# Optimization experiments

Measured on AMD Instinct MI355X. Metric: run time of the kernel, lower is better.

Reference implementation:

```python
import jax, jax.numpy as jnp
import numpy as np

NUM_EXPERTS = 64
TOP_K = 8
ALPHA = 0.001


def setup_inputs() -> dict:
    key = jax.random.key(0)
    k1, k2 = jax.random.split(key)
    hidden_states = jax.random.normal(k1, (16384, 2048), dtype=jnp.float32)
    # nn.Linear(D, E) weight has shape (E, D); init ~ N(0, 1/sqrt(D))
    weight = jax.random.normal(k2, (NUM_EXPERTS, 2048), dtype=jnp.float32) / jnp.sqrt(2048.0)
    return {"hidden_states": hidden_states, "weight": weight}


def reference(hidden_states, weight):
    # Router logits: (N, E)
    logits = jnp.einsum("nd,ed->ne", hidden_states, weight)
    scores = jax.nn.softmax(logits, axis=-1)

    # top-k (lax.top_k returns sorted values; torch used sorted=False, same set)
    topk_weights, topk_indices = jax.lax.top_k(scores, TOP_K)  # (N, K)
    topk_weights = topk_weights / jnp.sum(topk_weights, axis=-1, keepdims=True)

    # Aux load-balancing loss (training path). Instead of materializing a
    # (N, K, E) one-hot tensor, count tokens per expert with a scatter-add.
    num_tokens = hidden_states.shape[0]
    counts = jnp.zeros((NUM_EXPERTS,), dtype=jnp.float32).at[topk_indices.ravel()].add(1.0)
    tokens_per_expert = counts / (num_tokens * TOP_K)
    mean_prob = jnp.mean(scores, axis=0)  # (E,)
    aux_loss = ALPHA * NUM_EXPERTS * jnp.sum(tokens_per_expert * mean_prob)

    return topk_weights, topk_indices, aux_loss
```

## Files before the change

### kernel.cpp

```cpp
#include <hip/hip_runtime.h>
#include <hip/hip_bf16.h>

#define N_TOKENS 16384
#define DIM      2048
#define NEXP     64
#define TOPK     8
#define BK       32

__global__ __launch_bounds__(256) void gemm_kernel(const float* __restrict__ A,
                                                   const float* __restrict__ W,
                                                   float* __restrict__ out,
                                                   int k_len) {
    __shared__ float As[BK][260];
    __shared__ float Bs[BK][68];

    const int tid = threadIdx.x;
    const int r = tid >> 3;
    const int c = tid & 7;
    const int token_base = blockIdx.x * 256;
    const int k_start = blockIdx.y * k_len;
    out += (size_t)blockIdx.y * N_TOKENS * NEXP;

    float acc[8][8] = {};

    for (int k0 = k_start; k0 < k_start + k_len; k0 += BK) {
        #pragma unroll
        for (int l = 0; l < 8; ++l) {
            int slot = tid + l * 256;
            int row  = slot >> 3;
            int kq   = (slot & 7) * 4;
            float4 v = *(const float4*)(A + (size_t)(token_base + row) * DIM + k0 + kq);
            As[kq + 0][row] = v.x; As[kq + 1][row] = v.y;
            As[kq + 2][row] = v.z; As[kq + 3][row] = v.w;
        }
        #pragma unroll
        for (int l = 0; l < 2; ++l) {
            int slot = tid + l * 256;
            int row  = slot >> 3;
            int kq   = (slot & 7) * 4;
            float4 v = *(const float4*)(W + (size_t)row * DIM + k0 + kq);
            Bs[kq + 0][row] = v.x; Bs[kq + 1][row] = v.y;
            Bs[kq + 2][row] = v.z; Bs[kq + 3][row] = v.w;
        }
        __syncthreads();

        #pragma unroll 8
        for (int kk = 0; kk < BK; ++kk) {
            float4 a0 = *(const float4*)&As[kk][8 * r];
            float4 a1 = *(const float4*)&As[kk][8 * r + 4];
            float4 b0 = *(const float4*)&Bs[kk][8 * c];
            float4 b1 = *(const float4*)&Bs[kk][8 * c + 4];
            float a[8] = {a0.x, a0.y, a0.z, a0.w, a1.x, a1.y, a1.z, a1.w};
            float b[8] = {b0.x, b0.y, b0.z, b0.w, b1.x, b1.y, b1.z, b1.w};
            #pragma unroll
            for (int i = 0; i < 8; ++i)
                #pragma unroll
                for (int j = 0; j < 8; ++j)
                    acc[i][j] += a[i] * b[j];
        }
        __syncthreads();
    }

    #pragma unroll
    for (int i = 0; i < 8; ++i) {
        float* orow = out + (size_t)(token_base + 8 * r + i) * NEXP + 8 * c;
        *(float4*)(orow)     = make_float4(acc[i][0], acc[i][1], acc[i][2], acc[i][3]);
        *(float4*)(orow + 4) = make_float4(acc[i][4], acc[i][5], acc[i][6], acc[i][7]);
    }
}

__global__ __launch_bounds__(256) void topk_kernel(const float* __restrict__ logits,
                                                   int nslab,
                                                   float* __restrict__ out_w,
                                                   float* __restrict__ out_i,
                                                   float* __restrict__ cnt_ws,
                                                   float* __restrict__ sp_ws) {
    __shared__ float s_cnt[NEXP];
    __shared__ float s_sp[NEXP];
    if (threadIdx.x < NEXP) { s_cnt[threadIdx.x] = 0.f; s_sp[threadIdx.x] = 0.f; }
    __syncthreads();

    const int lane = threadIdx.x & 63;
    const int wave = blockIdx.x * 4 + (threadIdx.x >> 6);

    float sp  = 0.f;
    float cnt = 0.f;

    for (int t = wave; t < N_TOKENS; t += 4096) {
        float lg = 0.f;
        for (int s = 0; s < nslab; ++s)
            lg += logits[(size_t)s * N_TOKENS * NEXP + (size_t)t * NEXP + lane];

        float m = lg;
        #pragma unroll
        for (int off = 32; off; off >>= 1) m = fmaxf(m, __shfl_xor(m, off));
        float e = expf(lg - m);
        float ssum = e;
        #pragma unroll
        for (int off = 32; off; off >>= 1) ssum += __shfl_xor(ssum, off);
        float score = e / ssum;
        sp += score;

        int rank = 0;
        #pragma unroll
        for (int j = 0; j < 64; ++j) {
            float sj = __shfl(score, j);
            rank += (sj > score) || (sj == score && j < lane);
        }
        bool sel = rank < TOPK;

        float v = sel ? score : 0.f;
        #pragma unroll
        for (int off = 32; off; off >>= 1) v += __shfl_xor(v, off);

        if (sel) {
            out_w[(size_t)t * TOPK + rank] = score / v;
            out_i[(size_t)t * TOPK + rank] = (float)lane;
            cnt += 1.f;
        }
    }

    atomicAdd(&s_sp[lane], sp);
    atomicAdd(&s_cnt[lane], cnt);
    __syncthreads();
    if (threadIdx.x < 64)       atomicAdd(&cnt_ws[threadIdx.x], s_cnt[threadIdx.x]);
    else if (threadIdx.x < 128) atomicAdd(&sp_ws[threadIdx.x - 64], s_sp[threadIdx.x - 64]);
}

__global__ void finalize_kernel(const float* __restrict__ cnt_ws,
                                const float* __restrict__ sp_ws,
                                float* __restrict__ out_aux) {
    int lane = threadIdx.x;
    float v = (cnt_ws[lane] / (float)(N_TOKENS * TOPK)) *
              (sp_ws[lane] / (float)N_TOKENS);
    #pragma unroll
    for (int off = 32; off; off >>= 1) v += __shfl_xor(v, off);
    if (lane == 0) out_aux[0] = 0.001f * (float)NEXP * v;
}

extern "C" void kernel_launch(void* const* d_in, const int* in_sizes, int n_in,
                              void* d_out, int out_size, void* d_ws, size_t ws_size,
                              hipStream_t stream) {
    const float* A = (const float*)d_in[0];
    const float* W = (const float*)d_in[1];
    float* out = (float*)d_out;

    const size_t logits_elems = (size_t)N_TOKENS * NEXP;
    const size_t logits_bytes = logits_elems * sizeof(float);

    int nslab = 1;
    if (ws_size >= 8 * logits_bytes + 1024)      nslab = 8;
    else if (ws_size >= 4 * logits_bytes + 1024) nslab = 4;
    else if (ws_size >= 2 * logits_bytes + 1024) nslab = 2;

    float* l0     = (float*)d_ws;
    float* cnt_ws = (float*)((char*)d_ws + (size_t)nslab * logits_bytes);
    float* sp_ws  = cnt_ws + NEXP;

    hipMemsetAsync(cnt_ws, 0, 2 * NEXP * sizeof(float), stream);

    hipLaunchKernelGGL(gemm_kernel, dim3(N_TOKENS / 256, nslab), dim3(256), 0, stream,
                       A, W, l0, DIM / nslab);

    float* out_w = out;
    float* out_i = out + (size_t)N_TOKENS * TOPK;
    float* out_a = out + 2 * (size_t)N_TOKENS * TOPK;

    hipLaunchKernelGGL(topk_kernel, dim3(1024), dim3(256), 0, stream,
                       l0, nslab, out_w, out_i, cnt_ws, sp_ws);

    hipLaunchKernelGGL(finalize_kernel, dim3(1), dim3(64), 0, stream,
                       cnt_ws, sp_ws, out_a);
}
```

Baseline: 261.5 us.

## Enlarge GEMM token tile to 512 with padded LDS layout and deeper split-K

The GEMM block now covers 512 tokens with BK=16, and each thread computes a 16x8 accumulator tile, so every loaded weight value is reused across more rows. Shared-memory stores use a padded, grouped layout to cut bank conflicts, and global loads are issued into registers before the LDS writes. Split-K defaults to at least 4 slabs (up to 16) to keep the grid filling the GPU, and the top-k kernel sums the slabs with four independent accumulators. The cost is more register pressure from the 128 accumulators, plus more logits traffic and a larger workspace for the extra slabs; if the workspace is smaller than four slabs, the writes overrun it.

Result: slower. 272.5 us (+4.2%).

```diff
diff --git a/kernel.cpp b/kernel.cpp
--- a/kernel.cpp
+++ b/kernel.cpp
@@ -5,55 +5,80 @@
 #define DIM      2048
 #define NEXP     64
 #define TOPK     8
-#define BK       32
-
-__global__ __launch_bounds__(256) void gemm_kernel(const float* __restrict__ A,
-                                                   const float* __restrict__ W,
-                                                   float* __restrict__ out,
-                                                   int k_len) {
-    __shared__ float As[BK][260];
-    __shared__ float Bs[BK][68];
+#define BK       16
+#define TM       512
+#define APLANE   644
+#define BPLANE   100
+
+__global__ __launch_bounds__(256, 2) void gemm_kernel(const float* __restrict__ A,
+                                                      const float* __restrict__ W,
+                                                      float* __restrict__ out,
+                                                      int k_len) {
+    __shared__ float As[BK * APLANE];
+    __shared__ float Bs[BK * BPLANE];
 
     const int tid = threadIdx.x;
-    const int r = tid >> 3;
-    const int c = tid & 7;
-    const int token_base = blockIdx.x * 256;
+    const int tg  = tid >> 3;
+    const int cg  = tid & 7;
+    const int token_base = blockIdx.x * TM;
     const int k_start = blockIdx.y * k_len;
     out += (size_t)blockIdx.y * N_TOKENS * NEXP;
 
-    float acc[8][8] = {};
+    float acc[16][8] = {};
 
     for (int k0 = k_start; k0 < k_start + k_len; k0 += BK) {
+        float4 av[8];
         #pragma unroll
         for (int l = 0; l < 8; ++l) {
             int slot = tid + l * 256;
-            int row  = slot >> 3;
-            int kq   = (slot & 7) * 4;
-            float4 v = *(const float4*)(A + (size_t)(token_base + row) * DIM + k0 + kq);
-            As[kq + 0][row] = v.x; As[kq + 1][row] = v.y;
-            As[kq + 2][row] = v.z; As[kq + 3][row] = v.w;
-        }
-        #pragma unroll
-        for (int l = 0; l < 2; ++l) {
+            int row  = slot >> 2;
+            int kq   = (slot & 3) << 2;
+            av[l] = *(const float4*)(A + (size_t)(token_base + row) * DIM + k0 + kq);
+        }
+        float4 bv;
+        {
+            int row = tid >> 2;
+            int kq  = (tid & 3) << 2;
+            bv = *(const float4*)(W + (size_t)row * DIM + k0 + kq);
+        }
+
+        #pragma unroll
+        for (int l = 0; l < 8; ++l) {
             int slot = tid + l * 256;
-            int row  = slot >> 3;
-            int kq   = (slot & 7) * 4;
-            float4 v = *(const float4*)(W + (size_t)row * DIM + k0 + kq);
-            Bs[kq + 0][row] = v.x; Bs[kq + 1][row] = v.y;
-            Bs[kq + 2][row] = v.z; Bs[kq + 3][row] = v.w;
+            int row  = slot >> 2;
+            int kq   = (slot & 3) << 2;
+            float* dst = As + (row >> 4) * 20 + (row & 15);
+            dst[(kq + 0) * APLANE] = av[l].x;
+            dst[(kq + 1) * APLANE] = av[l].y;
+            dst[(kq + 2) * APLANE] = av[l].z;
+            dst[(kq + 3) * APLANE] = av[l].w;
+        }
+        {
+            int row = tid >> 2;
+            int kq  = (tid & 3) << 2;
+            float* dst = Bs + (row >> 3) * 12 + (row & 7);
+            dst[(kq + 0) * BPLANE] = bv.x;
+            dst[(kq + 1) * BPLANE] = bv.y;
+            dst[(kq + 2) * BPLANE] = bv.z;
+            dst[(kq + 3) * BPLANE] = bv.w;
         }
         __syncthreads();
 
-        #pragma unroll 8
+        #pragma unroll 4
         for (int kk = 0; kk < BK; ++kk) {
-            float4 a0 = *(const float4*)&As[kk][8 * r];
-            float4 a1 = *(const float4*)&As[kk][8 * r + 4];
-            float4 b0 = *(const float4*)&Bs[kk][8 * c];
-            float4 b1 = *(const float4*)&Bs[kk][8 * c + 4];
-            float a[8] = {a0.x, a0.y, a0.z, a0.w, a1.x, a1.y, a1.z, a1.w};
-            float b[8] = {b0.x, b0.y, b0.z, b0.w, b1.x, b1.y, b1.z, b1.w};
+            const float* ap = As + kk * APLANE + tg * 20;
+            const float* bp = Bs + kk * BPLANE + cg * 12;
+            float4 a0 = *(const float4*)(ap);
+            float4 a1 = *(const float4*)(ap + 4);
+            float4 a2 = *(const float4*)(ap + 8);
+            float4 a3 = *(const float4*)(ap + 12);
+            float4 b0 = *(const float4*)(bp);
+            float4 b1 = *(const float4*)(bp + 4);
+            float a[16] = {a0.x, a0.y, a0.z, a0.w, a1.x, a1.y, a1.z, a1.w,
+                           a2.x, a2.y, a2.z, a2.w, a3.x, a3.y, a3.z, a3.w};
+            float b[8]  = {b0.x, b0.y, b0.z, b0.w, b1.x, b1.y, b1.z, b1.w};
             #pragma unroll
-            for (int i = 0; i < 8; ++i)
+            for (int i = 0; i < 16; ++i)
                 #pragma unroll
                 for (int j = 0; j < 8; ++j)
                     acc[i][j] += a[i] * b[j];
@@ -62,8 +87,8 @@
     }
 
     #pragma unroll
-    for (int i = 0; i < 8; ++i) {
-        float* orow = out + (size_t)(token_base + 8 * r + i) * NEXP + 8 * c;
+    for (int i = 0; i < 16; ++i) {
+        float* orow = out + (size_t)(token_base + tg * 16 + i) * NEXP + cg * 8;
         *(float4*)(orow)     = make_float4(acc[i][0], acc[i][1], acc[i][2], acc[i][3]);
         *(float4*)(orow + 4) = make_float4(acc[i][4], acc[i][5], acc[i][6], acc[i][7]);
     }
@@ -82,14 +107,21 @@
 
     const int lane = threadIdx.x & 63;
     const int wave = blockIdx.x * 4 + (threadIdx.x >> 6);
+    const size_t slab_stride = (size_t)N_TOKENS * NEXP;
 
     float sp  = 0.f;
     float cnt = 0.f;
 
     for (int t = wave; t < N_TOKENS; t += 4096) {
-        float lg = 0.f;
-        for (int s = 0; s < nslab; ++s)
-            lg += logits[(size_t)s * N_TOKENS * NEXP + (size_t)t * NEXP + lane];
+        const float* p = logits + (size_t)t * NEXP + lane;
+        float s0 = 0.f, s1 = 0.f, s2 = 0.f, s3 = 0.f;
+        for (int s = 0; s < nslab; s += 4) {
+            s0 += p[(size_t)(s + 0) * slab_stride];
+            s1 += p[(size_t)(s + 1) * slab_stride];
+            s2 += p[(size_t)(s + 2) * slab_stride];
+            s3 += p[(size_t)(s + 3) * slab_stride];
+        }
+        float lg = (s0 + s1) + (s2 + s3);
 
         float m = lg;
         #pragma unroll
@@ -148,10 +180,9 @@
     const size_t logits_elems = (size_t)N_TOKENS * NEXP;
     const size_t logits_bytes = logits_elems * sizeof(float);
 
-    int nslab = 1;
-    if (ws_size >= 8 * logits_bytes + 1024)      nslab = 8;
-    else if (ws_size >= 4 * logits_bytes + 1024) nslab = 4;
-    else if (ws_size >= 2 * logits_bytes + 1024) nslab = 2;
+    int nslab = 4;
+    if (ws_size >= 16 * logits_bytes + 1024)     nslab = 16;
+    else if (ws_size >= 8 * logits_bytes + 1024) nslab = 8;
 
     float* l0     = (float*)d_ws;
     float* cnt_ws = (float*)((char*)d_ws + (size_t)nslab * logits_bytes);
@@ -159,7 +190,7 @@
 
     hipMemsetAsync(cnt_ws, 0, 2 * NEXP * sizeof(float), stream);
 
-    hipLaunchKernelGGL(gemm_kernel, dim3(N_TOKENS / 256, nslab), dim3(256), 0, stream,
+    hipLaunchKernelGGL(gemm_kernel, dim3(N_TOKENS / TM, nslab), dim3(256), 0, stream,
                        A, W, l0, DIM / nslab);
 
     float* out_w = out;
```

## Prefetch GEMM tiles into registers, raise split-K to 16 slabs, widen top-k grid

Applied to the files above, without the earlier changes.

The GEMM now loads the next K-tile into registers while the current tile is computed from shared memory, overlapping global latency with FMA work. BK is halved and launch bounds request 4 blocks per CU for occupancy. The split-K default rises from 8 to 16 slabs when the workspace allows, which gives more blocks but doubles the partial-logit traffic. The top-k kernel reduces slabs with four independent accumulators and launches twice as many blocks. The 4-way unrolled slab reduction assumes nslab is a multiple of 4, which the new host logic guarantees.

After: 282.8 us. +8.1%, slower.

```diff
diff --git a/kernel.cpp b/kernel.cpp
--- a/kernel.cpp
+++ b/kernel.cpp
@@ -5,46 +5,61 @@
 #define DIM      2048
 #define NEXP     64
 #define TOPK     8
-#define BK       32
+#define BK       16
+#define TM       256
+#define NSLAB    16
 
-__global__ __launch_bounds__(256) void gemm_kernel(const float* __restrict__ A,
-                                                   const float* __restrict__ W,
-                                                   float* __restrict__ out,
-                                                   int k_len) {
+__global__ __launch_bounds__(256, 4) void gemm_kernel(const float* __restrict__ A,
+                                                      const float* __restrict__ W,
+                                                      float* __restrict__ out,
+                                                      int k_len) {
     __shared__ float As[BK][260];
     __shared__ float Bs[BK][68];
 
     const int tid = threadIdx.x;
     const int r = tid >> 3;
     const int c = tid & 7;
-    const int token_base = blockIdx.x * 256;
+    const int token_base = blockIdx.x * TM;
     const int k_start = blockIdx.y * k_len;
     out += (size_t)blockIdx.y * N_TOKENS * NEXP;
 
+    const int arow = tid >> 2;
+    const int akq  = (tid & 3) << 2;
+    const float* aptr = A + (size_t)(token_base + arow) * DIM + akq;
+    const float* wptr = W + (size_t)arow * DIM + akq;
+
     float acc[8][8] = {};
+    float4 av[4], bv;
 
-    for (int k0 = k_start; k0 < k_start + k_len; k0 += BK) {
+    #pragma unroll
+    for (int l = 0; l < 4; ++l)
+        av[l] = *(const float4*)(aptr + (size_t)l * 64 * DIM + k_start);
+    bv = *(const float4*)(wptr + k_start);
+
+    const int n_iters = k_len / BK;
+    for (int it = 0; it < n_iters; ++it) {
         #pragma unroll
-        for (int l = 0; l < 8; ++l) {
-            int slot = tid + l * 256;
-            int row  = slot >> 3;
-            int kq   = (slot & 7) * 4;
-            float4 v = *(const float4*)(A + (size_t)(token_base + row) * DIM + k0 + kq);
-            As[kq + 0][row] = v.x; As[kq + 1][row] = v.y;
-            As[kq + 2][row] = v.z; As[kq + 3][row] = v.w;
+        for (int l = 0; l < 4; ++l) {
+            float* dst = &As[0][0] + akq * 260 + (arow + l * 64);
+            dst[0 * 260] = av[l].x; dst[1 * 260] = av[l].y;
+            dst[2 * 260] = av[l].z; dst[3 * 260] = av[l].w;
         }
-        #pragma unroll
-        for (int l = 0; l < 2; ++l) {
-            int slot = tid + l * 256;
-            int row  = slot >> 3;
-            int kq   = (slot & 7) * 4;
-            float4 v = *(const float4*)(W + (size_t)row * DIM + k0 + kq);
-            Bs[kq + 0][row] = v.x; Bs[kq + 1][row] = v.y;
-            Bs[kq + 2][row] = v.z; Bs[kq + 3][row] = v.w;
+        {
+            float* dst = &Bs[0][0] + akq * 68 + arow;
+            dst[0 * 68] = bv.x; dst[1 * 68] = bv.y;
+            dst[2 * 68] = bv.z; dst[3 * 68] = bv.w;
         }
         __syncthreads();
 
-        #pragma unroll 8
+        if (it + 1 < n_iters) {
+            int k0 = k_start + (it + 1) * BK;
+            #pragma unroll
+            for (int l = 0; l < 4; ++l)
+                av[l] = *(const float4*)(aptr + (size_t)l * 64 * DIM + k0);
+            bv = *(const float4*)(wptr + k0);
+        }
+
+        #pragma unroll 4
         for (int kk = 0; kk < BK; ++kk) {
             float4 a0 = *(const float4*)&As[kk][8 * r];
             float4 a1 = *(const float4*)&As[kk][8 * r + 4];
@@ -82,14 +97,21 @@
 
     const int lane = threadIdx.x & 63;
     const int wave = blockIdx.x * 4 + (threadIdx.x >> 6);
+    const size_t slab_stride = (size_t)N_TOKENS * NEXP;
 
     float sp  = 0.f;
     float cnt = 0.f;
 
-    for (int t = wave; t < N_TOKENS; t += 4096) {
-        float lg = 0.f;
-        for (int s = 0; s < nslab; ++s)
-            lg += logits[(size_t)s * N_TOKENS * NEXP + (size_t)t * NEXP + lane];
+    for (int t = wave; t < N_TOKENS; t += 8192) {
+        const float* p = logits + (size_t)t * NEXP + lane;
+        float s0 = 0.f, s1 = 0.f, s2 = 0.f, s3 = 0.f;
+        for (int s = 0; s < nslab; s += 4) {
+            s0 += p[(size_t)(s + 0) * slab_stride];
+            s1 += p[(size_t)(s + 1) * slab_stride];
+            s2 += p[(size_t)(s + 2) * slab_stride];
+            s3 += p[(size_t)(s + 3) * slab_stride];
+        }
+        float lg = (s0 + s1) + (s2 + s3);
 
         float m = lg;
         #pragma unroll
@@ -148,10 +170,9 @@
     const size_t logits_elems = (size_t)N_TOKENS * NEXP;
     const size_t logits_bytes = logits_elems * sizeof(float);
 
-    int nslab = 1;
-    if (ws_size >= 8 * logits_bytes + 1024)      nslab = 8;
-    else if (ws_size >= 4 * logits_bytes + 1024) nslab = 4;
-    else if (ws_size >= 2 * logits_bytes + 1024) nslab = 2;
+    int nslab = 4;
+    if (ws_size >= 16 * logits_bytes + 1024)     nslab = 16;
+    else if (ws_size >= 8 * logits_bytes + 1024) nslab = 8;
 
     float* l0     = (float*)d_ws;
     float* cnt_ws = (float*)((char*)d_ws + (size_t)nslab * logits_bytes);
@@ -159,14 +180,14 @@
 
     hipMemsetAsync(cnt_ws, 0, 2 * NEXP * sizeof(float), stream);
 
-    hipLaunchKernelGGL(gemm_kernel, dim3(N_TOKENS / 256, nslab), dim3(256), 0, stream,
+    hipLaunchKernelGGL(gemm_kernel, dim3(N_TOKENS / TM, nslab), dim3(256), 0, stream,
                        A, W, l0, DIM / nslab);
 
     float* out_w = out;
     float* out_i = out + (size_t)N_TOKENS * TOPK;
     float* out_a = out + 2 * (size_t)N_TOKENS * TOPK;
 
-    hipLaunchKernelGGL(topk_kernel, dim3(1024), dim3(256), 0, stream,
+    hipLaunchKernelGGL(topk_kernel, dim3(2048), dim3(256), 0, stream,
                        l0, nslab, out_w, out_i, cnt_ws, sp_ws);
 
     hipLaunchKernelGGL(finalize_kernel, dim3(1), dim3(64), 0, stream,
```
